# Kernel optimization log

Measured on AMD Instinct MI355X. Metric: run time of the kernel, lower is better.

The kernel has to match this reference:

```python
import jax, jax.numpy as jnp
import numpy as np


def _rx(state, theta, axis):
    # Apply RX(theta) to qubit at tensor axis `axis`. state: (B, 2,...,2) complex.
    half = theta * 0.5
    c = jnp.cos(half)
    s = jnp.sin(half)
    a0 = jnp.take(state, 0, axis=axis)
    a1 = jnp.take(state, 1, axis=axis)
    return jnp.stack([c * a0 - 1j * s * a1, c * a1 - 1j * s * a0], axis=axis)


def _cnot(state, w):
    # CNOT with control wire w (axis w+1), target wire w+1 (axis w+2).
    c_ax = w + 1
    s0 = jnp.take(state, 0, axis=c_ax)
    # after removing the control axis, the target axis index becomes c_ax
    s1 = jnp.flip(jnp.take(state, 1, axis=c_ax), axis=c_ax)
    return jnp.stack([s0, s1], axis=c_ax)


def _run_circuit(x, params):
    # x: (B, n) encoding angles; params: (depth, n) trainable RX angles.
    B, n = x.shape
    depth = params.shape[0]
    state = jnp.zeros((B,) + (2,) * n, jnp.complex64)
    state = state.at[(slice(None),) + (0,) * n].set(1.0 + 0.0j)
    # angle encoding: RX(x_w) on each wire
    for w in range(n):
        theta = x[:, w].reshape((B,) + (1,) * (n - 1))
        state = _rx(state, theta, w + 1)
    # variational layers: RX(param) per wire, then CNOT chain
    for d in range(depth):
        for w in range(n):
            state = _rx(state, params[d, w], w + 1)
        for w in range(n - 1):
            state = _cnot(state, w)
    probs = state.real ** 2 + state.imag ** 2  # (B, 2,...,2)
    ez = []
    for w in range(n):
        axes = tuple(a for a in range(1, n + 1) if a != w + 1)
        p = probs.sum(axes)  # (B, 2)
        ez.append(p[:, 0] - p[:, 1])  # <Z_w>
    return jnp.stack(ez, axis=1)  # (B, n)


def setup_inputs() -> dict:
    key = jax.random.key(0)
    k0, k1, k2, k3, k4 = jax.random.split(key, 5)
    seq_len, batch, input_dim = 256, 128, 64
    n_qubits, depth, hidden = 10, 2, 256
    inputs = jax.random.normal(k0, (seq_len, batch, input_dim), jnp.float32)
    mask = jax.random.randint(k1, (seq_len, batch), 0, 2).astype(jnp.int32)
    qparams = jax.random.normal(k2, (4, depth, n_qubits), jnp.float32)
    W = jax.random.normal(k3, (4, hidden, n_qubits), jnp.float32) / np.sqrt(n_qubits)
    b = jax.random.normal(k4, (4, hidden), jnp.float32) * 0.01
    return {"inputs": inputs, "mask": mask, "qparams": qparams, "W": W, "b": b}


def reference(inputs, mask, qparams, W, b):
    seq_len, batch, _ = inputs.shape
    n = qparams.shape[-1]
    hidden = W.shape[1]
    maskf = mask.astype(inputs.dtype)

    circuits4 = jax.vmap(_run_circuit, in_axes=(None, 0))  # over the 4 gates

    def step(carry, xm):
        hx, cx = carry
        x_t, m_t = xm
        q_in = jnp.concatenate([x_t, hx], axis=1)[:, :n]  # (B, n)
        z = circuits4(q_in, qparams)                      # (4, B, n)
        pre = jnp.einsum('gbn,ghn->gbh', z, W) + b[:, None, :]
        f = jax.nn.sigmoid(pre[0])
        i = jax.nn.sigmoid(pre[1])
        g = jnp.tanh(pre[2])
        o = jax.nn.sigmoid(pre[3])
        m = m_t[:, None]
        f = f * m + (1.0 - m)
        i = i * m
        g = g * m
        o = o * m + (1.0 - m)
        cx_new = f * cx + i * g
        hx_new = o * jnp.tanh(cx_new)
        return (hx_new, cx_new), hx_new

    h0 = jnp.zeros((batch, hidden), inputs.dtype)
    c0 = jnp.zeros((batch, hidden), inputs.dtype)
    (hx, cx), outputs = jax.lax.scan(jax.checkpoint(step), (h0, c0), (inputs, maskf))
    return outputs, (hx, cx)
```

## Files before the change

### kernel.cpp

```cpp
#include <hip/hip_runtime.h>

#define T_LEN 256
#define BATCH 128
#define NQ 10
#define HID 256
#define OUT_HX (T_LEN * BATCH * HID)
#define OUT_CX (OUT_HX + BATCH * HID)

#define KS  (-1.44269504089f)
#define KT2 (-2.88539008178f)

__global__ __launch_bounds__(256) void zker(
    const float* __restrict__ inputs,
    const float* __restrict__ qparams,
    float* __restrict__ zws)
{
  const int b   = blockIdx.x;
  const int tq  = blockIdx.y;
  const int tid = threadIdx.x;
  const int t   = tq * 64 + (tid >> 2);
  const int g   = tid & 3;

  const float sg = (g == 2) ? KT2 : KS;

  float th0[NQ], cth[NQ], sth[NQ];
#pragma unroll
  for (int k = 0; k < NQ; ++k) {
    th0[k]   = qparams[g * 2 * NQ + k];
    float t1 = qparams[g * 2 * NQ + NQ + k];
    sth[k] = __sinf(t1);
    cth[k] = __cosf(t1);
  }
  float cphi[NQ], sphi[NQ];
  const float* xp = inputs + (t * BATCH + b) * 64;
#pragma unroll
  for (int k = 0; k < NQ; ++k) {
    float ang = xp[k] + th0[k];
    sphi[k] = __sinf(ang);
    cphi[k] = __cosf(ang);
  }
  float* zout = zws + (b * T_LEN + t) * 40 + g;
#pragma unroll
  for (int w = 0; w < NQ; ++w) {
    float vI, vZ, vY, vX; int js;
    if (w == NQ - 1) { vI = 0.f; vZ = cth[NQ-1]; vY = sth[NQ-1]; vX = 0.f; js = NQ - 2; }
    else             { vI = 1.f; vZ = 0.f; vY = 0.f; vX = 0.f; js = w; }
#pragma unroll
    for (int j = js; j >= 0; --j) {
      float nI = cth[j] * (cphi[j+1] * vZ - sphi[j+1] * vY);
      float nZ = cth[j] * vI;
      float nY = sth[j] * vX;
      float nX = -sth[j] * (sphi[j+1] * vZ + cphi[j+1] * vY);
      vI = nI; vZ = nZ; vY = nY; vX = nX;
    }
    zout[w * 4] = (vI + cphi[0] * vZ - sphi[0] * vY) * sg;
  }
}

__global__ __launch_bounds__(512, 2) void scanker(
    const float* __restrict__ zws,
    const int*  __restrict__ mask,
    const float* __restrict__ W,
    const float* __restrict__ bias,
    float* __restrict__ out)
{
  const int b    = blockIdx.x;
  const int h0   = blockIdx.y * 64;
  const int tid  = threadIdx.x;
  const int lane = tid & 63;
  const int wavu = __builtin_amdgcn_readfirstlane(tid >> 6);
  const int h    = h0 + lane;

  __shared__ float cA[8][64];
  __shared__ float cW[8][64];

  float Wf[NQ], Wi[NQ], Wg[NQ], Wo[NQ];
#pragma unroll
  for (int n = 0; n < NQ; ++n) {
    Wf[n] = W[(0 * HID + h) * NQ + n];
    Wi[n] = W[(1 * HID + h) * NQ + n];
    Wg[n] = W[(2 * HID + h) * NQ + n];
    Wo[n] = W[(3 * HID + h) * NQ + n];
  }
  const float bf = bias[0 * HID + h] * KS;
  const float bi = bias[1 * HID + h] * KS;
  const float bg = bias[2 * HID + h] * KT2;
  const float bo = bias[3 * HID + h] * KS;

  const float* zb = zws + b * T_LEN * 40;

  float wv[32];
  float A = 1.f, Wc = 0.f;
#pragma unroll
  for (int k = 0; k < 32; ++k) {
    const int t = wavu * 32 + k;
    if (mask[t * BATCH + b]) {
      const float4* zrow = (const float4*)(zb + t * 40);
      float p0 = bf, p1 = bi, p2 = bg;
#pragma unroll
      for (int n = 0; n < NQ; ++n) {
        const float4 z = zrow[n];
        p0 = fmaf(z.x, Wf[n], p0);
        p1 = fmaf(z.y, Wi[n], p1);
        p2 = fmaf(z.z, Wg[n], p2);
      }
      const float a  = __builtin_amdgcn_rcpf(1.f + __builtin_amdgcn_exp2f(p0));
      const float ui = __builtin_amdgcn_rcpf(1.f + __builtin_amdgcn_exp2f(p1));
      const float ug = __builtin_amdgcn_rcpf(1.f + __builtin_amdgcn_exp2f(p2));
      const float wt = ui * fmaf(2.f, ug, -1.f);
      wv[k] = wt;
      Wc = fmaf(a, Wc, wt);
      A  = a * A;
    } else {
      wv[k] = 0.f;
    }
  }
  cA[wavu][lane] = A;
  cW[wavu][lane] = Wc;
  __syncthreads();

  float c = 0.f;
  for (int k = 0; k < wavu; ++k)
    c = fmaf(cA[k][lane], c, cW[k][lane]);

  float tc;
  {
    const float ec = __builtin_amdgcn_exp2f(c * KT2);
    tc = fmaf(2.f, __builtin_amdgcn_rcpf(1.f + ec), -1.f);
  }

  float hv = tc;
#pragma unroll
  for (int k = 0; k < 32; ++k) {
    const int t = wavu * 32 + k;
    if (mask[t * BATCH + b]) {
      const float4* zrow = (const float4*)(zb + t * 40);
      float p0 = bf, p3 = bo;
#pragma unroll
      for (int n = 0; n < NQ; ++n) {
        const float4 z = zrow[n];
        p0 = fmaf(z.x, Wf[n], p0);
        p3 = fmaf(z.w, Wo[n], p3);
      }
      const float a  = __builtin_amdgcn_rcpf(1.f + __builtin_amdgcn_exp2f(p0));
      const float uo = __builtin_amdgcn_rcpf(1.f + __builtin_amdgcn_exp2f(p3));
      c = fmaf(a, c, wv[k]);
      const float ec = __builtin_amdgcn_exp2f(c * KT2);
      tc = fmaf(2.f, __builtin_amdgcn_rcpf(1.f + ec), -1.f);
      hv = uo * tc;
    } else {
      hv = tc;
    }
    out[t * (BATCH * HID) + b * HID + h] = hv;
  }
  if (wavu == 7) {
    out[OUT_HX + b * HID + h] = hv;
    out[OUT_CX + b * HID + h] = c;
  }
}

extern "C" void kernel_launch(void* const* d_in, const int* in_sizes, int n_in,
                              void* d_out, int out_size, void* d_ws, size_t ws_size,
                              hipStream_t stream)
{
  int ii = 0, im = 1, iq = 2, iw = 3, ib = 4;
  for (int i = 0; i < n_in; ++i) {
    switch (in_sizes[i]) {
      case 2097152: ii = i; break;
      case 32768:   im = i; break;
      case 80:      iq = i; break;
      case 10240:   iw = i; break;
      case 1024:    ib = i; break;
      default: break;
    }
  }
  const float* inputs  = (const float*)d_in[ii];
  const int*   mask    = (const int*)d_in[im];
  const float* qparams = (const float*)d_in[iq];
  const float* W       = (const float*)d_in[iw];
  const float* bias    = (const float*)d_in[ib];
  float*       out     = (float*)d_out;
  float*       zws     = (float*)d_ws;

  zker<<<dim3(BATCH, 4), dim3(256), 0, stream>>>(inputs, qparams, zws);
  scanker<<<dim3(BATCH, 4), dim3(512), 0, stream>>>(zws, mask, W, bias, out);
}
```

Before: 116.6 us.

## Stage z rows and mask bits in LDS, skip masked steps in zker

The scan kernel now copies each batch's z workspace (40 KB) into shared memory and builds per-wave mask bitmasks with a ballot, replacing repeated global loads of z and mask. The second pass recomputes the i and g gates instead of holding a 32-entry register array, and occupancy is raised to 4 blocks per CU. zker now exits early for masked-out timesteps, skipping circuit evaluation whose results are never read. The trade-offs are 40 KB of LDS per block, which may cap residency below the requested 4, and extra ALU work in the second pass.

Measured after the change: 101.3 us. 1.15x faster.

```diff
diff --git a/kernel.cpp b/kernel.cpp
--- a/kernel.cpp
+++ b/kernel.cpp
@@ -12,6 +12,7 @@
 
 __global__ __launch_bounds__(256) void zker(
     const float* __restrict__ inputs,
+    const int*  __restrict__ mask,
     const float* __restrict__ qparams,
     float* __restrict__ zws)
 {
@@ -21,6 +22,8 @@
   const int t   = tq * 64 + (tid >> 2);
   const int g   = tid & 3;
 
+  if (mask[t * BATCH + b] == 0) return;
+
   const float sg = (g == 2) ? KT2 : KS;
 
   float th0[NQ], cth[NQ], sth[NQ];
@@ -57,7 +60,7 @@
   }
 }
 
-__global__ __launch_bounds__(512, 2) void scanker(
+__global__ __launch_bounds__(512, 4) void scanker(
     const float* __restrict__ zws,
     const int*  __restrict__ mask,
     const float* __restrict__ W,
@@ -71,8 +74,23 @@
   const int wavu = __builtin_amdgcn_readfirstlane(tid >> 6);
   const int h    = h0 + lane;
 
+  __shared__ float4 zl4[T_LEN * 10];
+  __shared__ unsigned int mbits[8];
   __shared__ float cA[8][64];
   __shared__ float cW[8][64];
+
+  {
+    const float4* zg = (const float4*)(zws + b * T_LEN * 40);
+    for (int i = tid; i < T_LEN * 10; i += 512) zl4[i] = zg[i];
+  }
+  if (tid < 256) {
+    const int mv = mask[tid * BATCH + b];
+    const unsigned long long bal = __ballot(mv != 0);
+    if ((tid & 63) == 0) {
+      mbits[(tid >> 6) * 2]     = (unsigned int)bal;
+      mbits[(tid >> 6) * 2 + 1] = (unsigned int)(bal >> 32);
+    }
+  }
 
   float Wf[NQ], Wi[NQ], Wg[NQ], Wo[NQ];
 #pragma unroll
@@ -87,32 +105,32 @@
   const float bg = bias[2 * HID + h] * KT2;
   const float bo = bias[3 * HID + h] * KS;
 
-  const float* zb = zws + b * T_LEN * 40;
-
-  float wv[32];
+  __syncthreads();
+
+  const unsigned int mb =
+      __builtin_amdgcn_readfirstlane(mbits[wavu]);
+
   float A = 1.f, Wc = 0.f;
-#pragma unroll
-  for (int k = 0; k < 32; ++k) {
-    const int t = wavu * 32 + k;
-    if (mask[t * BATCH + b]) {
-      const float4* zrow = (const float4*)(zb + t * 40);
-      float p0 = bf, p1 = bi, p2 = bg;
-#pragma unroll
-      for (int n = 0; n < NQ; ++n) {
-        const float4 z = zrow[n];
-        p0 = fmaf(z.x, Wf[n], p0);
-        p1 = fmaf(z.y, Wi[n], p1);
-        p2 = fmaf(z.z, Wg[n], p2);
+  {
+    unsigned int mrem = mb;
+    for (int k = 0; k < 32; ++k, mrem >>= 1) {
+      if (mrem & 1u) {
+        const int zt = (wavu * 32 + k) * 10;
+        float p0 = bf, p1 = bi, p2 = bg;
+#pragma unroll
+        for (int n = 0; n < NQ; ++n) {
+          const float4 z = zl4[zt + n];
+          p0 = fmaf(z.x, Wf[n], p0);
+          p1 = fmaf(z.y, Wi[n], p1);
+          p2 = fmaf(z.z, Wg[n], p2);
+        }
+        const float a  = __builtin_amdgcn_rcpf(1.f + __builtin_amdgcn_exp2f(p0));
+        const float ui = __builtin_amdgcn_rcpf(1.f + __builtin_amdgcn_exp2f(p1));
+        const float ug = __builtin_amdgcn_rcpf(1.f + __builtin_amdgcn_exp2f(p2));
+        const float wt = ui * fmaf(2.f, ug, -1.f);
+        Wc = fmaf(a, Wc, wt);
+        A  = a * A;
       }
-      const float a  = __builtin_amdgcn_rcpf(1.f + __builtin_amdgcn_exp2f(p0));
-      const float ui = __builtin_amdgcn_rcpf(1.f + __builtin_amdgcn_exp2f(p1));
-      const float ug = __builtin_amdgcn_rcpf(1.f + __builtin_amdgcn_exp2f(p2));
-      const float wt = ui * fmaf(2.f, ug, -1.f);
-      wv[k] = wt;
-      Wc = fmaf(a, Wc, wt);
-      A  = a * A;
-    } else {
-      wv[k] = 0.f;
     }
   }
   cA[wavu][lane] = A;
@@ -130,28 +148,34 @@
   }
 
   float hv = tc;
-#pragma unroll
-  for (int k = 0; k < 32; ++k) {
-    const int t = wavu * 32 + k;
-    if (mask[t * BATCH + b]) {
-      const float4* zrow = (const float4*)(zb + t * 40);
-      float p0 = bf, p3 = bo;
-#pragma unroll
-      for (int n = 0; n < NQ; ++n) {
-        const float4 z = zrow[n];
-        p0 = fmaf(z.x, Wf[n], p0);
-        p3 = fmaf(z.w, Wo[n], p3);
+  {
+    unsigned int mrem = mb;
+    for (int k = 0; k < 32; ++k, mrem >>= 1) {
+      const int t = wavu * 32 + k;
+      if (mrem & 1u) {
+        const int zt = t * 10;
+        float p0 = bf, p1 = bi, p2 = bg, p3 = bo;
+#pragma unroll
+        for (int n = 0; n < NQ; ++n) {
+          const float4 z = zl4[zt + n];
+          p0 = fmaf(z.x, Wf[n], p0);
+          p1 = fmaf(z.y, Wi[n], p1);
+          p2 = fmaf(z.z, Wg[n], p2);
+          p3 = fmaf(z.w, Wo[n], p3);
+        }
+        const float a  = __builtin_amdgcn_rcpf(1.f + __builtin_amdgcn_exp2f(p0));
+        const float ui = __builtin_amdgcn_rcpf(1.f + __builtin_amdgcn_exp2f(p1));
+        const float ug = __builtin_amdgcn_rcpf(1.f + __builtin_amdgcn_exp2f(p2));
+        const float uo = __builtin_amdgcn_rcpf(1.f + __builtin_amdgcn_exp2f(p3));
+        c = fmaf(a, c, ui * fmaf(2.f, ug, -1.f));
+        const float ec = __builtin_amdgcn_exp2f(c * KT2);
+        tc = fmaf(2.f, __builtin_amdgcn_rcpf(1.f + ec), -1.f);
+        hv = uo * tc;
+      } else {
+        hv = tc;
       }
-      const float a  = __builtin_amdgcn_rcpf(1.f + __builtin_amdgcn_exp2f(p0));
-      const float uo = __builtin_amdgcn_rcpf(1.f + __builtin_amdgcn_exp2f(p3));
-      c = fmaf(a, c, wv[k]);
-      const float ec = __builtin_amdgcn_exp2f(c * KT2);
-      tc = fmaf(2.f, __builtin_amdgcn_rcpf(1.f + ec), -1.f);
-      hv = uo * tc;
-    } else {
-      hv = tc;
-    }
-    out[t * (BATCH * HID) + b * HID + h] = hv;
+      out[t * (BATCH * HID) + b * HID + h] = hv;
+    }
   }
   if (wavu == 7) {
     out[OUT_HX + b * HID + h] = hv;
@@ -182,6 +206,6 @@
   float*       out     = (float*)d_out;
   float*       zws     = (float*)d_ws;
 
-  zker<<<dim3(BATCH, 4), dim3(256), 0, stream>>>(inputs, qparams, zws);
+  zker<<<dim3(BATCH, 4), dim3(256), 0, stream>>>(inputs, mask, qparams, zws);
   scanker<<<dim3(BATCH, 4), dim3(512), 0, stream>>>(zws, mask, W, bias, out);
 }
```
